# Kernel tuning notes

Hardware: AMD Instinct MI355X
Metric: run time of the kernel (lower is better)

The kernel has to match this reference:

```python
import jax, jax.numpy as jnp
import numpy as np

GRID = (32, 32)       # SOM grid shape
INPUT_DIM = 512
BATCH = 16384
TAU = 0.5             # softmax temperature
EPS = 1e-8


def setup_inputs() -> dict:
    key = jax.random.key(0)
    k1, k2 = jax.random.split(key)
    x = jax.random.normal(k1, (BATCH, INPUT_DIM), dtype=jnp.float32)
    # glorot_uniform for shape (*GRID, INPUT_DIM): fan_in = 32*32, fan_out = 512
    fan_in, fan_out = GRID[0] * GRID[1], INPUT_DIM
    limit = float(np.sqrt(6.0 / (fan_in + fan_out)))
    weights_map = jax.random.uniform(
        k2, (*GRID, INPUT_DIM), dtype=jnp.float32, minval=-limit, maxval=limit
    )
    return {"x": x, "weights_map": weights_map}


def reference(x, weights_map):
    """SoftSOM forward: squared distances -> per-dimension softmax -> soft reconstruction."""
    B, D = x.shape
    gh, gw = GRID
    w_flat = weights_map.reshape(gh * gw, D)  # [N, D]
    d2 = (
        jnp.sum(x * x, axis=-1, keepdims=True)           # [B,1]
        + jnp.sum(w_flat * w_flat, axis=-1)[None, :]     # [1,N]
        - 2.0 * (x @ w_flat.T)                           # [B,N]
    )
    logits = (-d2 / TAU).reshape(B, gh, gw)
    # per-dimension softmax: softmax along each grid axis, combined multiplicatively
    s_rows = jax.nn.softmax(logits, axis=1)   # softmax over grid dim 0
    s_cols = jax.nn.softmax(logits, axis=2)   # softmax over grid dim 1
    a = s_rows * s_cols
    a = a / (jnp.sum(a, axis=(1, 2), keepdims=True) + EPS)  # renormalize over grid
    # soft reconstruction: weighted sum of prototypes
    y = jnp.einsum("bij,ijd->bd", a, weights_map)  # [B, D]
    return y
```

## Files before the change

kernel.cpp:

```cpp
#include <hip/hip_runtime.h>
#include <hip/hip_bf16.h>
#include <stdint.h>

#define B_SZ 16384
#define D_SZ 512
#define N_SZ 1024

using f16x8 = __attribute__((ext_vector_type(8))) _Float16;
using f16x4 = __attribute__((ext_vector_type(4))) _Float16;
using f32x4 = __attribute__((ext_vector_type(4))) float;

typedef unsigned int u32_as1 __attribute__((address_space(1)));
typedef unsigned int u32_as3 __attribute__((address_space(3)));

__device__ __forceinline__ void gload16(const void* g, void* lds_base) {
    __builtin_amdgcn_global_load_lds((const u32_as1*)g, (u32_as3*)lds_base, 16, 0, 0);
}

__global__ __launch_bounds__(256) void prep_w(
    const float* __restrict__ W, _Float16* __restrict__ wh,
    _Float16* __restrict__ wt, float* __restrict__ ww) {
    const int n = blockIdx.x;
    const int t = threadIdx.x;
    __shared__ float part[4];
    const float2 v = *reinterpret_cast<const float2*>(&W[(size_t)n * D_SZ + t * 2]);
    _Float16 h0 = (_Float16)v.x, h1 = (_Float16)v.y;
    wh[(size_t)n * D_SZ + t * 2] = h0;
    wh[(size_t)n * D_SZ + t * 2 + 1] = h1;
    wt[(size_t)(t * 2) * N_SZ + n] = h0;
    wt[(size_t)(t * 2 + 1) * N_SZ + n] = h1;
    float s = v.x * v.x + v.y * v.y;
    for (int o = 32; o; o >>= 1) s += __shfl_xor(s, o);
    if ((t & 63) == 0) part[t >> 6] = s;
    __syncthreads();
    if (t == 0) ww[n] = part[0] + part[1] + part[2] + part[3];
}

__global__ __launch_bounds__(256, 2) void gemm1(
    const float* __restrict__ X, const _Float16* __restrict__ wh,
    const float* __restrict__ ww, float* __restrict__ L) {
    __shared__ _Float16 As[2 * 128 * 32];
    __shared__ _Float16 Bs[2 * 128 * 32];
    const int tid = threadIdx.x;
    const int wid = tid >> 6, lane = tid & 63;
    const int raw = blockIdx.y * 8 + blockIdx.x;
    const int wsw = (raw & 7) * 128 + (raw >> 3);
    const int bn0 = (wsw & 7) * 128;
    const int bm0 = (wsw >> 3) * 128;
    const int m0 = (wid >> 1) * 64, n0 = (wid & 1) * 64;
    const int rA = lane & 15;
    const int cbr = (lane >> 4) * 16;
    const int rswz = ((rA >> 1) & 3) << 4;

    const int ar = tid >> 1;
    const int ac = (tid & 1) * 16;
    const size_t xoff = (size_t)(bm0 + ar) * D_SZ + ac;
    const int aswz = ((ar >> 1) & 3) << 4;
    const int awo0 = ar * 64 + ((ac * 2) ^ aswz);
    const int awo1 = ar * 64 + ((ac * 2 + 16) ^ aswz);
    char* const As_b = (char*)As;
    char* const Bs_b = (char*)Bs;

    const int br0 = (wid * 2) * 16 + (lane >> 2);
    const int br1 = (wid * 2 + 1) * 16 + (lane >> 2);
    const int sg0 = ((lane & 3) ^ ((br0 >> 1) & 3)) * 8;
    const int sg1 = ((lane & 3) ^ ((br1 >> 1) & 3)) * 8;
    const int bdst0 = (wid * 2) * 1024;
    const int bdst1 = (wid * 2 + 1) * 1024;

    f32x4 acc[4][4];
    for (int mi = 0; mi < 4; ++mi)
        for (int ni = 0; ni < 4; ++ni) acc[mi][ni] = (f32x4){0.f, 0.f, 0.f, 0.f};

    {
        const float4 x0 = *reinterpret_cast<const float4*>(&X[xoff]);
        const float4 x1 = *reinterpret_cast<const float4*>(&X[xoff + 4]);
        const float4 x2 = *reinterpret_cast<const float4*>(&X[xoff + 8]);
        const float4 x3 = *reinterpret_cast<const float4*>(&X[xoff + 12]);
        gload16(&wh[(size_t)(bn0 + br0) * D_SZ + sg0], Bs_b + bdst0);
        gload16(&wh[(size_t)(bn0 + br1) * D_SZ + sg1], Bs_b + bdst1);
        f16x8 h0 = {(_Float16)x0.x, (_Float16)x0.y, (_Float16)x0.z, (_Float16)x0.w,
                    (_Float16)x1.x, (_Float16)x1.y, (_Float16)x1.z, (_Float16)x1.w};
        f16x8 h1 = {(_Float16)x2.x, (_Float16)x2.y, (_Float16)x2.z, (_Float16)x2.w,
                    (_Float16)x3.x, (_Float16)x3.y, (_Float16)x3.z, (_Float16)x3.w};
        *reinterpret_cast<f16x8*>(As_b + awo0) = h0;
        *reinterpret_cast<f16x8*>(As_b + awo1) = h1;
    }
    __syncthreads();

    int cur = 0;
    for (int kt = 0; kt < 16; ++kt) {
        const int nxt = cur ^ 1;
        float4 x0, x1, x2, x3;
        if (kt < 15) {
            const int gk = (kt + 1) * 32;
            x0 = *reinterpret_cast<const float4*>(&X[xoff + gk]);
            x1 = *reinterpret_cast<const float4*>(&X[xoff + gk + 4]);
            x2 = *reinterpret_cast<const float4*>(&X[xoff + gk + 8]);
            x3 = *reinterpret_cast<const float4*>(&X[xoff + gk + 12]);
            gload16(&wh[(size_t)(bn0 + br0) * D_SZ + gk + sg0], Bs_b + nxt * 8192 + bdst0);
            gload16(&wh[(size_t)(bn0 + br1) * D_SZ + gk + sg1], Bs_b + nxt * 8192 + bdst1);
        }
        f16x8 af[4], bf[4];
        for (int mi = 0; mi < 4; ++mi)
            af[mi] = *reinterpret_cast<const f16x8*>(
                As_b + cur * 8192 + (m0 + mi * 16 + rA) * 64 + (cbr ^ rswz));
        for (int ni = 0; ni < 4; ++ni)
            bf[ni] = *reinterpret_cast<const f16x8*>(
                Bs_b + cur * 8192 + (n0 + ni * 16 + rA) * 64 + (cbr ^ rswz));
        for (int mi = 0; mi < 4; ++mi)
            for (int ni = 0; ni < 4; ++ni)
                acc[mi][ni] = __builtin_amdgcn_mfma_f32_16x16x32_f16(af[mi], bf[ni], acc[mi][ni], 0, 0, 0);
        if (kt < 15) {
            f16x8 h0 = {(_Float16)x0.x, (_Float16)x0.y, (_Float16)x0.z, (_Float16)x0.w,
                        (_Float16)x1.x, (_Float16)x1.y, (_Float16)x1.z, (_Float16)x1.w};
            f16x8 h1 = {(_Float16)x2.x, (_Float16)x2.y, (_Float16)x2.z, (_Float16)x2.w,
                        (_Float16)x3.x, (_Float16)x3.y, (_Float16)x3.z, (_Float16)x3.w};
            *reinterpret_cast<f16x8*>(As_b + nxt * 8192 + awo0) = h0;
            *reinterpret_cast<f16x8*>(As_b + nxt * 8192 + awo1) = h1;
        }
        __syncthreads();
        cur = nxt;
    }
    for (int mi = 0; mi < 4; ++mi)
        for (int ni = 0; ni < 4; ++ni) {
            const int nn = bn0 + n0 + ni * 16 + rA;
            const float wwn = ww[nn];
            const int bb = bm0 + m0 + mi * 16 + (lane >> 4) * 4;
            const f32x4 a = acc[mi][ni];
            for (int r = 0; r < 4; ++r)
                L[(size_t)(bb + r) * N_SZ + nn] = 4.f * a[r] - 2.f * wwn;
        }
}

__global__ __launch_bounds__(256) void softsm(float* __restrict__ L) {
    __shared__ float4 cpart[4][8];
    __shared__ float4 spart[4][8];
    __shared__ float Tp[4];
    const int t = threadIdx.x;
    const int w = t >> 6, lane = t & 63;
    const int g8 = t & 7;
    const size_t row = blockIdx.x;
    const float4 v = *reinterpret_cast<const float4*>(&L[row * N_SZ + (size_t)t * 4]);
    float l0 = v.x, l1 = v.y, l2 = v.z, l3 = v.w;

    float rm = fmaxf(fmaxf(l0, l1), fmaxf(l2, l3));
    rm = fmaxf(rm, __shfl_xor(rm, 1));
    rm = fmaxf(rm, __shfl_xor(rm, 2));
    rm = fmaxf(rm, __shfl_xor(rm, 4));
    float c0 = l0, c1 = l1, c2 = l2, c3 = l3;
    for (int m = 8; m <= 32; m <<= 1) {
        c0 = fmaxf(c0, __shfl_xor(c0, m));
        c1 = fmaxf(c1, __shfl_xor(c1, m));
        c2 = fmaxf(c2, __shfl_xor(c2, m));
        c3 = fmaxf(c3, __shfl_xor(c3, m));
    }
    if (lane < 8) cpart[w][lane] = make_float4(c0, c1, c2, c3);
    __syncthreads();
    {
        const float4 q0 = cpart[0][g8], q1 = cpart[1][g8], q2 = cpart[2][g8], q3 = cpart[3][g8];
        c0 = fmaxf(fmaxf(q0.x, q1.x), fmaxf(q2.x, q3.x));
        c1 = fmaxf(fmaxf(q0.y, q1.y), fmaxf(q2.y, q3.y));
        c2 = fmaxf(fmaxf(q0.z, q1.z), fmaxf(q2.z, q3.z));
        c3 = fmaxf(fmaxf(q0.w, q1.w), fmaxf(q2.w, q3.w));
    }
    const float er0 = expf(l0 - rm), er1 = expf(l1 - rm), er2 = expf(l2 - rm), er3 = expf(l3 - rm);
    const float ec0 = expf(l0 - c0), ec1 = expf(l1 - c1), ec2 = expf(l2 - c2), ec3 = expf(l3 - c3);
    float rs = er0 + er1 + er2 + er3;
    rs += __shfl_xor(rs, 1); rs += __shfl_xor(rs, 2); rs += __shfl_xor(rs, 4);
    float s0 = ec0, s1 = ec1, s2 = ec2, s3 = ec3;
    for (int m = 8; m <= 32; m <<= 1) {
        s0 += __shfl_xor(s0, m);
        s1 += __shfl_xor(s1, m);
        s2 += __shfl_xor(s2, m);
        s3 += __shfl_xor(s3, m);
    }
    if (lane < 8) spart[w][lane] = make_float4(s0, s1, s2, s3);
    __syncthreads();
    {
        const float4 q0 = spart[0][g8], q1 = spart[1][g8], q2 = spart[2][g8], q3 = spart[3][g8];
        s0 = (q0.x + q1.x) + (q2.x + q3.x);
        s1 = (q0.y + q1.y) + (q2.y + q3.y);
        s2 = (q0.z + q1.z) + (q2.z + q3.z);
        s3 = (q0.w + q1.w) + (q2.w + q3.w);
    }
    const float irs = 1.f / rs;
    const float tt0 = er0 * ec0 * irs / s0;
    const float tt1 = er1 * ec1 * irs / s1;
    const float tt2 = er2 * ec2 * irs / s2;
    const float tt3 = er3 * ec3 * irs / s3;
    float sT = (tt0 + tt1) + (tt2 + tt3);
    for (int m = 1; m <= 32; m <<= 1) sT += __shfl_xor(sT, m);
    if (lane == 0) Tp[w] = sT;
    __syncthreads();
    const float T = (Tp[0] + Tp[1]) + (Tp[2] + Tp[3]);
    const float inv = 1.f / (T + 1e-8f);
    f16x4 o = {(_Float16)(tt0 * inv), (_Float16)(tt1 * inv),
               (_Float16)(tt2 * inv), (_Float16)(tt3 * inv)};
    char* out = (char*)L + (row >> 1) * 8192 + 4096 + (row & 1) * 2048 + (size_t)t * 8;
    *reinterpret_cast<f16x4*>(out) = o;
}

__global__ __launch_bounds__(256, 2) void gemm2(
    const char* __restrict__ aBytes, const _Float16* __restrict__ wt,
    float* __restrict__ Y) {
    __shared__ _Float16 As[2 * 128 * 32];
    __shared__ _Float16 Bs[2 * 128 * 32];
    const int tid = threadIdx.x;
    const int wid = tid >> 6, lane = tid & 63;
    const int raw = blockIdx.y * 4 + blockIdx.x;
    const int wsw = (raw & 7) * 64 + (raw >> 3);
    const int bn0 = (wsw & 3) * 128;
    const int bm0 = (wsw >> 2) * 128;
    const int m0 = (wid >> 1) * 64, n0 = (wid & 1) * 64;
    const int rA = lane & 15;
    const int cbr = (lane >> 4) * 16;
    const int rswz = ((rA >> 1) & 3) << 4;

    const int br0 = (wid * 2) * 16 + (lane >> 2);
    const int br1 = (wid * 2 + 1) * 16 + (lane >> 2);
    const int sg0 = ((lane & 3) ^ ((br0 >> 1) & 3)) * 8;
    const int sg1 = ((lane & 3) ^ ((br1 >> 1) & 3)) * 8;
    const int bdst0 = (wid * 2) * 1024;
    const int bdst1 = (wid * 2 + 1) * 1024;
    char* const As_b = (char*)As;
    char* const Bs_b = (char*)Bs;
    const int ab0 = bm0 + br0, ab1 = bm0 + br1;
    const size_t abase0 = (size_t)(ab0 >> 1) * 8192 + 4096 + (size_t)(ab0 & 1) * 2048;
    const size_t abase1 = (size_t)(ab1 >> 1) * 8192 + 4096 + (size_t)(ab1 & 1) * 2048;

    f32x4 acc[4][4];
    for (int mi = 0; mi < 4; ++mi)
        for (int ni = 0; ni < 4; ++ni) acc[mi][ni] = (f32x4){0.f, 0.f, 0.f, 0.f};

    gload16(aBytes + abase0 + (size_t)sg0 * 2, As_b + bdst0);
    gload16(aBytes + abase1 + (size_t)sg1 * 2, As_b + bdst1);
    gload16(&wt[(size_t)(bn0 + br0) * N_SZ + sg0], Bs_b + bdst0);
    gload16(&wt[(size_t)(bn0 + br1) * N_SZ + sg1], Bs_b + bdst1);
    __syncthreads();

    int cur = 0;
    for (int kt = 0; kt < 32; ++kt) {
        const int nxt = cur ^ 1;
        if (kt < 31) {
            const int gk = (kt + 1) * 32;
            gload16(aBytes + abase0 + (size_t)(gk + sg0) * 2, As_b + nxt * 8192 + bdst0);
            gload16(aBytes + abase1 + (size_t)(gk + sg1) * 2, As_b + nxt * 8192 + bdst1);
            gload16(&wt[(size_t)(bn0 + br0) * N_SZ + gk + sg0], Bs_b + nxt * 8192 + bdst0);
            gload16(&wt[(size_t)(bn0 + br1) * N_SZ + gk + sg1], Bs_b + nxt * 8192 + bdst1);
        }
        f16x8 af[4], bf[4];
        for (int mi = 0; mi < 4; ++mi)
            af[mi] = *reinterpret_cast<const f16x8*>(
                As_b + cur * 8192 + (m0 + mi * 16 + rA) * 64 + (cbr ^ rswz));
        for (int ni = 0; ni < 4; ++ni)
            bf[ni] = *reinterpret_cast<const f16x8*>(
                Bs_b + cur * 8192 + (n0 + ni * 16 + rA) * 64 + (cbr ^ rswz));
        for (int mi = 0; mi < 4; ++mi)
            for (int ni = 0; ni < 4; ++ni)
                acc[mi][ni] = __builtin_amdgcn_mfma_f32_16x16x32_f16(af[mi], bf[ni], acc[mi][ni], 0, 0, 0);
        __syncthreads();
        cur = nxt;
    }
    for (int mi = 0; mi < 4; ++mi)
        for (int ni = 0; ni < 4; ++ni) {
            const int dd = bn0 + n0 + ni * 16 + rA;
            const int bb = bm0 + m0 + mi * 16 + (lane >> 4) * 4;
            const f32x4 a = acc[mi][ni];
            for (int r = 0; r < 4; ++r)
                Y[(size_t)(bb + r) * D_SZ + dd] = a[r];
        }
}

extern "C" void kernel_launch(void* const* d_in, const int* in_sizes, int n_in,
                              void* d_out, int out_size, void* d_ws, size_t ws_size,
                              hipStream_t stream) {
    (void)in_sizes; (void)n_in; (void)out_size; (void)ws_size;
    const float* X = (const float*)d_in[0];
    const float* W = (const float*)d_in[1];
    float* Y = (float*)d_out;
    char* ws = (char*)d_ws;

    float* L = (float*)ws;
    _Float16* wh = (_Float16*)(ws + (size_t)64 * 1024 * 1024);
    _Float16* wt = wh + (size_t)N_SZ * D_SZ;
    float* ww = (float*)(wt + (size_t)N_SZ * D_SZ);

    prep_w<<<N_SZ, 256, 0, stream>>>(W, wh, wt, ww);
    gemm1<<<dim3(N_SZ / 128, B_SZ / 128), 256, 0, stream>>>(X, wh, ww, L);
    softsm<<<B_SZ, 256, 0, stream>>>(L);
    gemm2<<<dim3(D_SZ / 128, B_SZ / 128), 256, 0, stream>>>((const char*)L, wt, Y);
}
```

Before: 114.4 us.

## Pre-convert X to fp16, load via LDS DMA, simplify softmax, raise occupancy

Adds a prep_x kernel that converts X to fp16 once, so gemm1 can stage both operands with global_load_lds instead of loading fp32 rows and converting them in registers every K step. The softmax kernel now uses a single max across the whole row, valid for both the row-wise and column-wise softmaxes, so one set of exponentials replaces two and the product becomes u*u. It also switches to fast __expf and rcp intrinsics and remaps rows to a strided block order. Both GEMMs raise launch bounds to 3 blocks per CU. The cost is an extra kernel launch plus a write and read of a 16 MB fp16 copy of X, and some loss of precision from the fast math and the shared max.

After: 105.5 us. 1.08x faster.

```diff
diff --git a/kernel.cpp b/kernel.cpp
--- a/kernel.cpp
+++ b/kernel.cpp
@@ -36,8 +36,18 @@
     if (t == 0) ww[n] = part[0] + part[1] + part[2] + part[3];
 }
 
-__global__ __launch_bounds__(256, 2) void gemm1(
-    const float* __restrict__ X, const _Float16* __restrict__ wh,
+__global__ __launch_bounds__(256) void prep_x(
+    const float* __restrict__ X, _Float16* __restrict__ xh) {
+    const size_t idx = ((size_t)blockIdx.x * 256 + threadIdx.x) * 8;
+    const float4 a = *reinterpret_cast<const float4*>(&X[idx]);
+    const float4 b = *reinterpret_cast<const float4*>(&X[idx + 4]);
+    f16x8 h = {(_Float16)a.x, (_Float16)a.y, (_Float16)a.z, (_Float16)a.w,
+               (_Float16)b.x, (_Float16)b.y, (_Float16)b.z, (_Float16)b.w};
+    *reinterpret_cast<f16x8*>(&xh[idx]) = h;
+}
+
+__global__ __launch_bounds__(256, 3) void gemm1(
+    const _Float16* __restrict__ xh, const _Float16* __restrict__ wh,
     const float* __restrict__ ww, float* __restrict__ L) {
     __shared__ _Float16 As[2 * 128 * 32];
     __shared__ _Float16 Bs[2 * 128 * 32];
@@ -52,52 +62,32 @@
     const int cbr = (lane >> 4) * 16;
     const int rswz = ((rA >> 1) & 3) << 4;
 
-    const int ar = tid >> 1;
-    const int ac = (tid & 1) * 16;
-    const size_t xoff = (size_t)(bm0 + ar) * D_SZ + ac;
-    const int aswz = ((ar >> 1) & 3) << 4;
-    const int awo0 = ar * 64 + ((ac * 2) ^ aswz);
-    const int awo1 = ar * 64 + ((ac * 2 + 16) ^ aswz);
-    char* const As_b = (char*)As;
-    char* const Bs_b = (char*)Bs;
-
     const int br0 = (wid * 2) * 16 + (lane >> 2);
     const int br1 = (wid * 2 + 1) * 16 + (lane >> 2);
     const int sg0 = ((lane & 3) ^ ((br0 >> 1) & 3)) * 8;
     const int sg1 = ((lane & 3) ^ ((br1 >> 1) & 3)) * 8;
     const int bdst0 = (wid * 2) * 1024;
     const int bdst1 = (wid * 2 + 1) * 1024;
+    char* const As_b = (char*)As;
+    char* const Bs_b = (char*)Bs;
 
     f32x4 acc[4][4];
     for (int mi = 0; mi < 4; ++mi)
         for (int ni = 0; ni < 4; ++ni) acc[mi][ni] = (f32x4){0.f, 0.f, 0.f, 0.f};
 
-    {
-        const float4 x0 = *reinterpret_cast<const float4*>(&X[xoff]);
-        const float4 x1 = *reinterpret_cast<const float4*>(&X[xoff + 4]);
-        const float4 x2 = *reinterpret_cast<const float4*>(&X[xoff + 8]);
-        const float4 x3 = *reinterpret_cast<const float4*>(&X[xoff + 12]);
-        gload16(&wh[(size_t)(bn0 + br0) * D_SZ + sg0], Bs_b + bdst0);
-        gload16(&wh[(size_t)(bn0 + br1) * D_SZ + sg1], Bs_b + bdst1);
-        f16x8 h0 = {(_Float16)x0.x, (_Float16)x0.y, (_Float16)x0.z, (_Float16)x0.w,
-                    (_Float16)x1.x, (_Float16)x1.y, (_Float16)x1.z, (_Float16)x1.w};
-        f16x8 h1 = {(_Float16)x2.x, (_Float16)x2.y, (_Float16)x2.z, (_Float16)x2.w,
-                    (_Float16)x3.x, (_Float16)x3.y, (_Float16)x3.z, (_Float16)x3.w};
-        *reinterpret_cast<f16x8*>(As_b + awo0) = h0;
-        *reinterpret_cast<f16x8*>(As_b + awo1) = h1;
-    }
+    gload16(&xh[(size_t)(bm0 + br0) * D_SZ + sg0], As_b + bdst0);
+    gload16(&xh[(size_t)(bm0 + br1) * D_SZ + sg1], As_b + bdst1);
+    gload16(&wh[(size_t)(bn0 + br0) * D_SZ + sg0], Bs_b + bdst0);
+    gload16(&wh[(size_t)(bn0 + br1) * D_SZ + sg1], Bs_b + bdst1);
     __syncthreads();
 
     int cur = 0;
     for (int kt = 0; kt < 16; ++kt) {
         const int nxt = cur ^ 1;
-        float4 x0, x1, x2, x3;
         if (kt < 15) {
             const int gk = (kt + 1) * 32;
-            x0 = *reinterpret_cast<const float4*>(&X[xoff + gk]);
-            x1 = *reinterpret_cast<const float4*>(&X[xoff + gk + 4]);
-            x2 = *reinterpret_cast<const float4*>(&X[xoff + gk + 8]);
-            x3 = *reinterpret_cast<const float4*>(&X[xoff + gk + 12]);
+            gload16(&xh[(size_t)(bm0 + br0) * D_SZ + gk + sg0], As_b + nxt * 8192 + bdst0);
+            gload16(&xh[(size_t)(bm0 + br1) * D_SZ + gk + sg1], As_b + nxt * 8192 + bdst1);
             gload16(&wh[(size_t)(bn0 + br0) * D_SZ + gk + sg0], Bs_b + nxt * 8192 + bdst0);
             gload16(&wh[(size_t)(bn0 + br1) * D_SZ + gk + sg1], Bs_b + nxt * 8192 + bdst1);
         }
@@ -111,14 +101,6 @@
         for (int mi = 0; mi < 4; ++mi)
             for (int ni = 0; ni < 4; ++ni)
                 acc[mi][ni] = __builtin_amdgcn_mfma_f32_16x16x32_f16(af[mi], bf[ni], acc[mi][ni], 0, 0, 0);
-        if (kt < 15) {
-            f16x8 h0 = {(_Float16)x0.x, (_Float16)x0.y, (_Float16)x0.z, (_Float16)x0.w,
-                        (_Float16)x1.x, (_Float16)x1.y, (_Float16)x1.z, (_Float16)x1.w};
-            f16x8 h1 = {(_Float16)x2.x, (_Float16)x2.y, (_Float16)x2.z, (_Float16)x2.w,
-                        (_Float16)x3.x, (_Float16)x3.y, (_Float16)x3.z, (_Float16)x3.w};
-            *reinterpret_cast<f16x8*>(As_b + nxt * 8192 + awo0) = h0;
-            *reinterpret_cast<f16x8*>(As_b + nxt * 8192 + awo1) = h1;
-        }
         __syncthreads();
         cur = nxt;
     }
@@ -134,46 +116,30 @@
 }
 
 __global__ __launch_bounds__(256) void softsm(float* __restrict__ L) {
-    __shared__ float4 cpart[4][8];
     __shared__ float4 spart[4][8];
+    __shared__ float mpart[4];
     __shared__ float Tp[4];
     const int t = threadIdx.x;
     const int w = t >> 6, lane = t & 63;
     const int g8 = t & 7;
-    const size_t row = blockIdx.x;
+    const int bid = blockIdx.x;
+    const size_t row = (size_t)((bid & 7) * 2048 + (bid >> 3));
     const float4 v = *reinterpret_cast<const float4*>(&L[row * N_SZ + (size_t)t * 4]);
-    float l0 = v.x, l1 = v.y, l2 = v.z, l3 = v.w;
-
-    float rm = fmaxf(fmaxf(l0, l1), fmaxf(l2, l3));
-    rm = fmaxf(rm, __shfl_xor(rm, 1));
-    rm = fmaxf(rm, __shfl_xor(rm, 2));
-    rm = fmaxf(rm, __shfl_xor(rm, 4));
-    float c0 = l0, c1 = l1, c2 = l2, c3 = l3;
-    for (int m = 8; m <= 32; m <<= 1) {
-        c0 = fmaxf(c0, __shfl_xor(c0, m));
-        c1 = fmaxf(c1, __shfl_xor(c1, m));
-        c2 = fmaxf(c2, __shfl_xor(c2, m));
-        c3 = fmaxf(c3, __shfl_xor(c3, m));
-    }
-    if (lane < 8) cpart[w][lane] = make_float4(c0, c1, c2, c3);
-    __syncthreads();
-    {
-        const float4 q0 = cpart[0][g8], q1 = cpart[1][g8], q2 = cpart[2][g8], q3 = cpart[3][g8];
-        c0 = fmaxf(fmaxf(q0.x, q1.x), fmaxf(q2.x, q3.x));
-        c1 = fmaxf(fmaxf(q0.y, q1.y), fmaxf(q2.y, q3.y));
-        c2 = fmaxf(fmaxf(q0.z, q1.z), fmaxf(q2.z, q3.z));
-        c3 = fmaxf(fmaxf(q0.w, q1.w), fmaxf(q2.w, q3.w));
-    }
-    const float er0 = expf(l0 - rm), er1 = expf(l1 - rm), er2 = expf(l2 - rm), er3 = expf(l3 - rm);
-    const float ec0 = expf(l0 - c0), ec1 = expf(l1 - c1), ec2 = expf(l2 - c2), ec3 = expf(l3 - c3);
-    float rs = er0 + er1 + er2 + er3;
+
+    float m = fmaxf(fmaxf(v.x, v.y), fmaxf(v.z, v.w));
+    for (int o = 32; o; o >>= 1) m = fmaxf(m, __shfl_xor(m, o));
+    if (lane == 0) mpart[w] = m;
+    __syncthreads();
+    m = fmaxf(fmaxf(mpart[0], mpart[1]), fmaxf(mpart[2], mpart[3]));
+
+    const float u0 = __expf(v.x - m), u1 = __expf(v.y - m);
+    const float u2 = __expf(v.z - m), u3 = __expf(v.w - m);
+    float rs = (u0 + u1) + (u2 + u3);
     rs += __shfl_xor(rs, 1); rs += __shfl_xor(rs, 2); rs += __shfl_xor(rs, 4);
-    float s0 = ec0, s1 = ec1, s2 = ec2, s3 = ec3;
-    for (int m = 8; m <= 32; m <<= 1) {
-        s0 += __shfl_xor(s0, m);
-        s1 += __shfl_xor(s1, m);
-        s2 += __shfl_xor(s2, m);
-        s3 += __shfl_xor(s3, m);
+    float s0 = u0, s1 = u1, s2 = u2, s3 = u3;
+    for (int o = 8; o <= 32; o <<= 1) {
+        s0 += __shfl_xor(s0, o); s1 += __shfl_xor(s1, o);
+        s2 += __shfl_xor(s2, o); s3 += __shfl_xor(s3, o);
     }
     if (lane < 8) spart[w][lane] = make_float4(s0, s1, s2, s3);
     __syncthreads();
@@ -184,24 +150,24 @@
         s2 = (q0.z + q1.z) + (q2.z + q3.z);
         s3 = (q0.w + q1.w) + (q2.w + q3.w);
     }
-    const float irs = 1.f / rs;
-    const float tt0 = er0 * ec0 * irs / s0;
-    const float tt1 = er1 * ec1 * irs / s1;
-    const float tt2 = er2 * ec2 * irs / s2;
-    const float tt3 = er3 * ec3 * irs / s3;
-    float sT = (tt0 + tt1) + (tt2 + tt3);
-    for (int m = 1; m <= 32; m <<= 1) sT += __shfl_xor(sT, m);
+    const float irs = __builtin_amdgcn_rcpf(rs);
+    const float t0 = u0 * u0 * irs * __builtin_amdgcn_rcpf(s0);
+    const float t1 = u1 * u1 * irs * __builtin_amdgcn_rcpf(s1);
+    const float t2 = u2 * u2 * irs * __builtin_amdgcn_rcpf(s2);
+    const float t3 = u3 * u3 * irs * __builtin_amdgcn_rcpf(s3);
+    float sT = (t0 + t1) + (t2 + t3);
+    for (int o = 1; o <= 32; o <<= 1) sT += __shfl_xor(sT, o);
     if (lane == 0) Tp[w] = sT;
     __syncthreads();
     const float T = (Tp[0] + Tp[1]) + (Tp[2] + Tp[3]);
-    const float inv = 1.f / (T + 1e-8f);
-    f16x4 o = {(_Float16)(tt0 * inv), (_Float16)(tt1 * inv),
-               (_Float16)(tt2 * inv), (_Float16)(tt3 * inv)};
+    const float inv = __builtin_amdgcn_rcpf(T + 1e-8f);
+    f16x4 o16 = {(_Float16)(t0 * inv), (_Float16)(t1 * inv),
+                 (_Float16)(t2 * inv), (_Float16)(t3 * inv)};
     char* out = (char*)L + (row >> 1) * 8192 + 4096 + (row & 1) * 2048 + (size_t)t * 8;
-    *reinterpret_cast<f16x4*>(out) = o;
-}
-
-__global__ __launch_bounds__(256, 2) void gemm2(
+    *reinterpret_cast<f16x4*>(out) = o16;
+}
+
+__global__ __launch_bounds__(256, 3) void gemm2(
     const char* __restrict__ aBytes, const _Float16* __restrict__ wt,
     float* __restrict__ Y) {
     __shared__ _Float16 As[2 * 128 * 32];
@@ -285,9 +251,11 @@
     _Float16* wh = (_Float16*)(ws + (size_t)64 * 1024 * 1024);
     _Float16* wt = wh + (size_t)N_SZ * D_SZ;
     float* ww = (float*)(wt + (size_t)N_SZ * D_SZ);
+    _Float16* xh = (_Float16*)((char*)ww + 4096);
 
     prep_w<<<N_SZ, 256, 0, stream>>>(W, wh, wt, ww);
-    gemm1<<<dim3(N_SZ / 128, B_SZ / 128), 256, 0, stream>>>(X, wh, ww, L);
+    prep_x<<<(B_SZ * D_SZ) / (256 * 8), 256, 0, stream>>>(X, xh);
+    gemm1<<<dim3(N_SZ / 128, B_SZ / 128), 256, 0, stream>>>(xh, wh, ww, L);
     softsm<<<B_SZ, 256, 0, stream>>>(L);
     gemm2<<<dim3(D_SZ / 128, B_SZ / 128), 256, 0, stream>>>((const char*)L, wt, Y);
 }
```
